# Performance work log

Hardware: AMD Instinct MI355X
Metric: run time of the kernel (lower is better)

Reference implementation:

```python
import jax, jax.numpy as jnp
import numpy as np

H = 1024
NH = 16
HD = H // NH

def setup_inputs() -> dict:
    key = jax.random.key(0)
    ks = jax.random.split(key, 8)
    s = 1.0 / np.sqrt(H)
    hidden_states = jax.random.normal(ks[0], (2, 2048, H), dtype=jnp.float32)
    attention_mask = jnp.zeros((2, 1, 1, 2048), dtype=jnp.float32)
    Wq = jax.random.uniform(ks[1], (H, H), jnp.float32, -s, s)
    bq = jax.random.uniform(ks[2], (H,), jnp.float32, -s, s)
    Wk = jax.random.uniform(ks[3], (H, H), jnp.float32, -s, s)
    bk = jax.random.uniform(ks[4], (H,), jnp.float32, -s, s)
    Wv = jax.random.uniform(ks[5], (H, H), jnp.float32, -s, s)
    bv = jax.random.uniform(ks[6], (H,), jnp.float32, -s, s)
    return {"hidden_states": hidden_states, "attention_mask": attention_mask,
            "Wq": Wq, "bq": bq, "Wk": Wk, "bk": bk, "Wv": Wv, "bv": bv}

def _split_heads(x):
    B, L, _ = x.shape
    return x.reshape(B, L, NH, HD).transpose(0, 2, 1, 3)  # [B, nh, L, hd]

def reference(hidden_states, attention_mask, Wq, bq, Wk, bk, Wv, bv):
    # QKV projections (nn.Linear: x @ W.T + b)
    Q = _split_heads(hidden_states @ Wq.T + bq)
    K = _split_heads(hidden_states @ Wk.T + bk)
    V = _split_heads(hidden_states @ Wv.T + bv)
    scale = 1.0 / np.sqrt(HD)
    scores = jnp.einsum('bhqd,bhkd->bhqk', Q, K) * scale  # [B, nh, L, L]
    scores = scores + attention_mask
    probs = jax.nn.softmax(scores, axis=-1)  # dropout in eval mode = identity
    context = jnp.einsum('bhqk,bhkd->bhqd', probs, V)
    B, _, L, _ = context.shape
    return context.transpose(0, 2, 1, 3).reshape(B, L, H)
```

## Files before the change

### kernel.cpp

```cpp
#include <hip/hip_runtime.h>
#include <math.h>
#include <stdint.h>

#define H_DIM 1024
#define NH 16
#define HD 64
#define B_DIM 2
#define L_DIM 2048
#define M_TOT (B_DIM * L_DIM)

typedef __bf16 bf16_t;
typedef __bf16 bf16x8 __attribute__((ext_vector_type(8)));
typedef __bf16 bf16x4 __attribute__((ext_vector_type(4)));
typedef float  f32x4  __attribute__((ext_vector_type(4)));

#define AS1 const __attribute__((address_space(1))) void*
#define AS3 __attribute__((address_space(3))) void*

__global__ __launch_bounds__(256)
void cast_all(const float* __restrict__ x,
              const float* __restrict__ Wq, const float* __restrict__ Wk,
              const float* __restrict__ Wv, bf16_t* __restrict__ dst)
{
    const size_t idx = ((size_t)blockIdx.x * 256 + threadIdx.x) * 4;
    const float* src;
    size_t off;
    if (idx < (size_t)M_TOT * H_DIM) { src = x; off = idx; }
    else {
        size_t j = idx - (size_t)M_TOT * H_DIM;
        int z = (int)(j >> 20);
        off = j & ((1u << 20) - 1);
        src = (z == 0) ? Wq : (z == 1) ? Wk : Wv;
    }
    const float4 v = *(const float4*)(src + off);
    bf16x4 o;
    o[0] = (bf16_t)v.x; o[1] = (bf16_t)v.y;
    o[2] = (bf16_t)v.z; o[3] = (bf16_t)v.w;
    *(bf16x4*)(dst + idx) = o;
}

__global__ __launch_bounds__(256, 1)
void qkv_mfma(const bf16_t* __restrict__ xb, const bf16_t* __restrict__ wb,
              const float* __restrict__ bq, const float* __restrict__ bk,
              const float* __restrict__ bv,
              bf16_t* __restrict__ qb, bf16_t* __restrict__ kb,
              bf16_t* __restrict__ vt)
{
    __shared__ bf16_t As0[128 * 32];
    __shared__ bf16_t As1[128 * 32];
    __shared__ bf16_t As2[128 * 32];
    __shared__ bf16_t Bs0[3][128 * 32];
    __shared__ bf16_t Bs1[3][128 * 32];
    __shared__ bf16_t Bs2[3][128 * 32];

    const int tid = threadIdx.x;
    const int n   = blockIdx.x;
    const int bn  = (n & 7) * 128;
    const int bm  = (n >> 3) * 128;

    const int wave = tid >> 6;
    const int lane = tid & 63;
    const int lc   = lane & 15;
    const int quad = lane >> 4;
    const int wm   = wave >> 1;
    const int wn   = wave & 1;

    f32x4 acc[3][4][4];
    #pragma unroll
    for (int z = 0; z < 3; ++z)
        #pragma unroll
        for (int i = 0; i < 4; ++i)
            #pragma unroll
            for (int j = 0; j < 4; ++j)
                acc[z][i][j] = (f32x4){0.f, 0.f, 0.f, 0.f};

    const int srow = tid >> 2;
    const int sseg = tid & 3;
    const bf16_t* gA = xb + (size_t)(bm + srow) * H_DIM + (sseg ^ (srow & 3)) * 8;
    const bf16_t* gB = wb + (size_t)(bn + srow) * H_DIM + (sseg ^ (srow & 3)) * 8;
    const int woff = wave * 1024;

    auto stage = [&](int k0, bf16_t* A_, bf16_t (*B_)[128 * 32]) {
        __builtin_amdgcn_global_load_lds((AS1)(gA + k0),
            (AS3)((char*)A_ + woff), 16, 0, 0);
        __builtin_amdgcn_global_load_lds((AS1)(gA + k0 + (size_t)64 * H_DIM),
            (AS3)((char*)A_ + woff + 4096), 16, 0, 0);
        #pragma unroll
        for (int z = 0; z < 3; ++z) {
            const bf16_t* g = gB + (size_t)z * H_DIM * H_DIM + k0;
            __builtin_amdgcn_global_load_lds((AS1)(g),
                (AS3)((char*)B_[z] + woff), 16, 0, 0);
            __builtin_amdgcn_global_load_lds((AS1)(g + (size_t)64 * H_DIM),
                (AS3)((char*)B_[z] + woff + 4096), 16, 0, 0);
        }
    };

    const int slot = (quad ^ (lc & 3)) * 8;
    auto compute = [&](const bf16_t* A_, const bf16_t (*B_)[128 * 32]) {
        bf16x8 a[4];
        #pragma unroll
        for (int mi = 0; mi < 4; ++mi)
            a[mi] = *(const bf16x8*)(A_ + (wm * 64 + mi * 16 + lc) * 32 + slot);
        #pragma unroll
        for (int z = 0; z < 3; ++z) {
            bf16x8 b[4];
            #pragma unroll
            for (int ni = 0; ni < 4; ++ni)
                b[ni] = *(const bf16x8*)(B_[z] + (wn * 64 + ni * 16 + lc) * 32 + slot);
            #pragma unroll
            for (int mi = 0; mi < 4; ++mi)
                #pragma unroll
                for (int ni = 0; ni < 4; ++ni)
                    acc[z][mi][ni] = __builtin_amdgcn_mfma_f32_16x16x32_bf16(
                        a[mi], b[ni], acc[z][mi][ni], 0, 0, 0);
        }
    };

    auto step = [&](int kk, bf16_t* cA, bf16_t (*cB)[128 * 32],
                    bf16_t* nA, bf16_t (*nB)[128 * 32], bool doStage) {
        __builtin_amdgcn_s_waitcnt(0x0F78);
        __builtin_amdgcn_s_barrier();
        if (doStage) stage((kk + 2) * 32, nA, nB);
        compute(cA, cB);
    };

    stage(0,  As0, Bs0);
    stage(32, As1, Bs1);
    #pragma unroll 1
    for (int t = 0; t < 10; ++t) {
        const int kk = t * 3;
        step(kk,     As0, Bs0, As2, Bs2, true);
        step(kk + 1, As1, Bs1, As0, Bs0, true);
        step(kk + 2, As2, Bs2, As1, Bs1, true);
    }
    step(30, As0, Bs0, As2, Bs2, false);
    __builtin_amdgcn_s_waitcnt(0x0F70);
    __builtin_amdgcn_s_barrier();
    compute(As1, Bs1);

    const int nb = bn + wn * 64;
    #pragma unroll
    for (int z = 0; z < 3; ++z) {
        const float* bias = (z == 0) ? bq : (z == 1) ? bk : bv;
        float biasv[4];
        #pragma unroll
        for (int ni = 0; ni < 4; ++ni) biasv[ni] = bias[nb + ni * 16 + lc];

        #pragma unroll
        for (int mi = 0; mi < 4; ++mi) {
            const int m0 = bm + wm * 64 + mi * 16 + quad * 4;
            if (z == 2) {
                const int b_ = m0 >> 11;
                const int l0 = m0 & 2047;
                #pragma unroll
                for (int ni = 0; ni < 4; ++ni) {
                    const int nn = nb + ni * 16 + lc;
                    const int h = nn >> 6, d = nn & 63;
                    bf16x4 pk;
                    #pragma unroll
                    for (int r = 0; r < 4; ++r)
                        pk[r] = (bf16_t)(acc[z][mi][ni][r] + biasv[ni]);
                    *(bf16x4*)(vt + (((size_t)(b_ * NH + h)) * HD + d) * L_DIM + l0) = pk;
                }
            } else {
                bf16_t* dst = (z == 0) ? qb : kb;
                #pragma unroll
                for (int r = 0; r < 4; ++r) {
                    const int m  = m0 + r;
                    const int b_ = m >> 11;
                    const int l  = m & 2047;
                    #pragma unroll
                    for (int ni = 0; ni < 4; ++ni) {
                        const int nn = nb + ni * 16 + lc;
                        const int h = nn >> 6, d = nn & 63;
                        dst[(((size_t)(b_ * NH + h)) * L_DIM + l) * HD + d] =
                            (bf16_t)(acc[z][mi][ni][r] + biasv[ni]);
                    }
                }
            }
        }
    }
}

#define EXP_C   0.180336879f
#define LOG2E   1.442695041f
#define EXP_SH  11.541560327f

__device__ __forceinline__ void attn_tile32(
    int kbase, bool pre,
    const bf16_t* curK, const bf16_t* curV,
    bf16_t* nxtK, bf16_t* nxtV,
    const bf16_t* gKw, const bf16_t* gVw, int wo,
    bf16_t* Ps, const float* mrow, int lc, int quad,
    const bf16x8 (&bQ)[2][2], f32x4 (&o)[2][4], float (&rs)[2])
{
    __builtin_amdgcn_s_waitcnt(0x0F70);
    __builtin_amdgcn_s_barrier();

    const int e = lc & 7;

    bf16x8 kf[2][2];
    #pragma unroll
    for (int ni = 0; ni < 2; ++ni) {
        const bf16_t* p = curK + (ni * 16 + lc) * 64;
        kf[ni][0] = *(const bf16x8*)(p + ((quad ^ e) << 3));
        kf[ni][1] = *(const bf16x8*)(p + (((quad ^ e) ^ 4) << 3));
    }

    if (pre) {
        const int nk = kbase + 32;
        #pragma unroll
        for (int i = 0; i < 2; ++i) {
            __builtin_amdgcn_global_load_lds(
                (AS1)(gKw + (size_t)nk * 64 + i * 512),
                (AS3)(nxtK + wo + i * 512), 16, 0, 0);
            __builtin_amdgcn_global_load_lds(
                (AS1)(gVw + nk + (size_t)i * 32768),
                (AS3)(nxtV + wo + i * 512), 16, 0, 0);
        }
    }

    float mvs[2][4];
    #pragma unroll
    for (int ni = 0; ni < 2; ++ni) {
        const float4 mv = *(const float4*)(mrow + kbase + ni * 16 + quad * 4);
        mvs[ni][0] = mv.x * LOG2E - EXP_SH;
        mvs[ni][1] = mv.y * LOG2E - EXP_SH;
        mvs[ni][2] = mv.z * LOG2E - EXP_SH;
        mvs[ni][3] = mv.w * LOG2E - EXP_SH;
    }

    #pragma unroll
    for (int f = 0; f < 2; ++f) {
        f32x4 s[2];
        #pragma unroll
        for (int ni = 0; ni < 2; ++ni) {
            f32x4 t = (f32x4){0.f, 0.f, 0.f, 0.f};
            t = __builtin_amdgcn_mfma_f32_16x16x32_bf16(kf[ni][0], bQ[f][0], t, 0, 0, 0);
            t = __builtin_amdgcn_mfma_f32_16x16x32_bf16(kf[ni][1], bQ[f][1], t, 0, 0, 0);
            s[ni] = t;
        }
        float acc = 0.f;
        #pragma unroll
        for (int ni = 0; ni < 2; ++ni) {
            bf16x4 pk;
            #pragma unroll
            for (int r = 0; r < 4; ++r) {
                const float p = __builtin_amdgcn_exp2f(s[ni][r] * EXP_C + mvs[ni][r]);
                acc += p;
                pk[r] = (bf16_t)p;
            }
            const int c = f * 4 + ni * 2 + (quad >> 1);
            *(bf16x4*)(Ps + lc * 64 + ((c ^ e) << 3) + ((quad & 1) << 2)) = pk;
        }
        rs[f] += acc;
    }

    bf16x8 vf[4];
    const int e2 = lc >> 1;
    #pragma unroll
    for (int dg = 0; dg < 4; ++dg) {
        const int p  = dg * 8 + (lc >> 1);
        const int ch = (((lc & 1) << 2) + quad) ^ e2;
        vf[dg] = *(const bf16x8*)(curV + p * 64 + (ch << 3));
    }

    #pragma unroll
    for (int f = 0; f < 2; ++f) {
        const int c = f * 4 + quad;
        const bf16x8 bP = *(const bf16x8*)(Ps + lc * 64 + ((c ^ e) << 3));
        #pragma unroll
        for (int dg = 0; dg < 4; ++dg)
            o[f][dg] = __builtin_amdgcn_mfma_f32_16x16x32_bf16(vf[dg], bP, o[f][dg], 0, 0, 0);
    }
}

__global__ __launch_bounds__(128, 4)
void attn_mfma(const bf16_t* __restrict__ qb, const bf16_t* __restrict__ kb,
               const bf16_t* __restrict__ vt, const float* __restrict__ mask,
               float* __restrict__ out, float* __restrict__ o1,
               float* __restrict__ l0, float* __restrict__ l1)
{
    __shared__ bf16_t Ks0[32 * 64];
    __shared__ bf16_t Ks1[32 * 64];
    __shared__ bf16_t Vs0[32 * 64];
    __shared__ bf16_t Vs1[32 * 64];
    __shared__ bf16_t Ps[2][16 * 64];

    const int tid  = threadIdx.x;
    const int wave = tid >> 6;
    const int lane = tid & 63;
    const int lc   = lane & 15;
    const int quad = lane >> 4;
    const int rl   = lane >> 3;
    const int sg   = lane & 7;

    const int n    = blockIdx.x;
    const int bh   = (n & 7) * 4 + ((n >> 3) & 3);
    const int q0   = ((n >> 5) & 31) * 64 + wave * 32;
    const int kh   = (n >> 10) & 1;
    const int k0   = kh << 10;
    const int b_   = bh >> 4;
    const int h    = bh & 15;

    bf16_t* Psw = Ps[wave];

    bf16x8 bQ[2][2];
    #pragma unroll
    for (int f = 0; f < 2; ++f) {
        const bf16_t* Qp = qb + ((size_t)bh * L_DIM + q0 + f * 16 + lc) * HD + quad * 8;
        bQ[f][0] = *(const bf16x8*)(Qp);
        bQ[f][1] = *(const bf16x8*)(Qp + 32);
    }

    const bf16_t* Kbase = kb + (size_t)bh * L_DIM * HD;
    const bf16_t* Vbase = vt + (size_t)bh * HD * L_DIM;
    const float*  mrow  = mask + (size_t)b_ * L_DIM + k0;

    const int cV = sg ^ rl;
    const bf16_t* gKw = Kbase + (size_t)(k0 + rl) * 64 + (sg ^ rl) * 8
                      + (size_t)wave * 1024;
    const bf16_t* gVw = Vbase + k0 + (size_t)(rl * 2 + (cV >> 2)) * L_DIM
                      + (cV & 3) * 8 + (size_t)wave * 65536;
    const int wo = wave * 1024;

    f32x4 o[2][4];
    #pragma unroll
    for (int f = 0; f < 2; ++f)
        #pragma unroll
        for (int dg = 0; dg < 4; ++dg) o[f][dg] = (f32x4){0.f, 0.f, 0.f, 0.f};
    float rs[2] = {0.f, 0.f};

    #pragma unroll
    for (int i = 0; i < 2; ++i) {
        __builtin_amdgcn_global_load_lds(
            (AS1)(gKw + i * 512),
            (AS3)(Ks0 + wo + i * 512), 16, 0, 0);
        __builtin_amdgcn_global_load_lds(
            (AS1)(gVw + (size_t)i * 32768),
            (AS3)(Vs0 + wo + i * 512), 16, 0, 0);
    }

    #pragma unroll 1
    for (int t2 = 0; t2 < 16; ++t2) {
        const int kb0 = t2 * 64;
        attn_tile32(kb0,      true,     Ks0, Vs0, Ks1, Vs1, gKw, gVw, wo, Psw,
                    mrow, lc, quad, bQ, o, rs);
        attn_tile32(kb0 + 32, t2 < 15,  Ks1, Vs1, Ks0, Vs0, gKw, gVw, wo, Psw,
                    mrow, lc, quad, bQ, o, rs);
    }

    float* obase = (kh == 0) ? out : o1;
    float* lbase = (kh == 0) ? l0  : l1;
    #pragma unroll
    for (int f = 0; f < 2; ++f) {
        float l = rs[f];
        l += __shfl_xor(l, 16);
        l += __shfl_xor(l, 32);
        if (quad == 0)
            lbase[(size_t)bh * L_DIM + q0 + f * 16 + lc] = l;
        float* orow = obase + ((size_t)(b_ * L_DIM + q0 + f * 16 + lc)) * H_DIM
                    + h * HD + quad * 4;
        #pragma unroll
        for (int dg = 0; dg < 4; ++dg)
            *(f32x4*)(orow + dg * 16) = o[f][dg];
    }
}

__global__ __launch_bounds__(256)
void attn_combine(const float* __restrict__ o1,
                  const float* __restrict__ l0, const float* __restrict__ l1,
                  float* __restrict__ out)
{
    const size_t idx = ((size_t)blockIdx.x * 256 + threadIdx.x) * 4;
    const int m   = (int)(idx >> 10);
    const int col = (int)(idx & 1023);
    const int b_  = m >> 11;
    const int q   = m & 2047;
    const int h   = col >> 6;
    const size_t lidx = ((size_t)(b_ * NH + h)) * L_DIM + q;
    const float inv = 1.0f / (l0[lidx] + l1[lidx]);
    f32x4 a = *(const f32x4*)(out + idx);
    const f32x4 b = *(const f32x4*)(o1 + idx);
    a = (a + b) * inv;
    *(f32x4*)(out + idx) = a;
}

extern "C" void kernel_launch(void* const* d_in, const int* in_sizes, int n_in,
                              void* d_out, int out_size, void* d_ws, size_t ws_size,
                              hipStream_t stream) {
    const float* hidden = (const float*)d_in[0];
    const float* mask   = (const float*)d_in[1];
    const float* Wq     = (const float*)d_in[2];
    const float* bq     = (const float*)d_in[3];
    const float* Wk     = (const float*)d_in[4];
    const float* bk     = (const float*)d_in[5];
    const float* Wv     = (const float*)d_in[6];
    const float* bv     = (const float*)d_in[7];
    float* out = (float*)d_out;

    const size_t XN = (size_t)M_TOT * H_DIM;
    const size_t WN = (size_t)3 * H_DIM * H_DIM;
    bf16_t* xwb = (bf16_t*)d_ws;
    bf16_t* qb  = xwb + XN + WN;
    bf16_t* kb  = qb + XN;
    bf16_t* vt  = kb + XN;
    float*  o1  = (float*)(vt + XN);
    float*  l0  = o1 + XN;
    float*  l1  = l0 + (size_t)B_DIM * NH * L_DIM;

    cast_all<<<(int)((XN + WN) / 1024), 256, 0, stream>>>(hidden, Wq, Wk, Wv, xwb);

    qkv_mfma<<<256, 256, 0, stream>>>(xwb, xwb + XN, bq, bk, bv, qb, kb, vt);

    attn_mfma<<<2048, 128, 0, stream>>>(qb, kb, vt, mask, out, o1, l0, l1);

    attn_combine<<<4096, 256, 0, stream>>>(o1, l0, l1, out);
}
```

Measured before the change: 177.5 us.

## Widen attention blocks to four waves sharing K/V tiles and LDS mask

New measurement: 172.2 us. 1.03x faster.

```diff
diff --git a/kernel.cpp b/kernel.cpp
--- a/kernel.cpp
+++ b/kernel.cpp
@@ -191,7 +191,7 @@
     const bf16_t* curK, const bf16_t* curV,
     bf16_t* nxtK, bf16_t* nxtV,
     const bf16_t* gKw, const bf16_t* gVw, int wo,
-    bf16_t* Ps, const float* mrow, int lc, int quad,
+    bf16_t* Ps, const float* mvsL, int lc, int quad,
     const bf16x8 (&bQ)[2][2], f32x4 (&o)[2][4], float (&rs)[2])
 {
     __builtin_amdgcn_s_waitcnt(0x0F70);
@@ -209,30 +209,23 @@
 
     if (pre) {
         const int nk = kbase + 32;
-        #pragma unroll
-        for (int i = 0; i < 2; ++i) {
-            __builtin_amdgcn_global_load_lds(
-                (AS1)(gKw + (size_t)nk * 64 + i * 512),
-                (AS3)(nxtK + wo + i * 512), 16, 0, 0);
-            __builtin_amdgcn_global_load_lds(
-                (AS1)(gVw + nk + (size_t)i * 32768),
-                (AS3)(nxtV + wo + i * 512), 16, 0, 0);
-        }
-    }
-
-    float mvs[2][4];
-    #pragma unroll
-    for (int ni = 0; ni < 2; ++ni) {
-        const float4 mv = *(const float4*)(mrow + kbase + ni * 16 + quad * 4);
-        mvs[ni][0] = mv.x * LOG2E - EXP_SH;
-        mvs[ni][1] = mv.y * LOG2E - EXP_SH;
-        mvs[ni][2] = mv.z * LOG2E - EXP_SH;
-        mvs[ni][3] = mv.w * LOG2E - EXP_SH;
-    }
+        __builtin_amdgcn_global_load_lds(
+            (AS1)(gKw + (size_t)nk * 64),
+            (AS3)(nxtK + wo), 16, 0, 0);
+        __builtin_amdgcn_global_load_lds(
+            (AS1)(gVw + nk),
+            (AS3)(nxtV + wo), 16, 0, 0);
+    }
+
+    f32x4 mvs[2];
+    #pragma unroll
+    for (int ni = 0; ni < 2; ++ni)
+        mvs[ni] = *(const f32x4*)(mvsL + kbase + ni * 16 + quad * 4);
 
     #pragma unroll
     for (int f = 0; f < 2; ++f) {
         f32x4 s[2];
+        __builtin_amdgcn_s_setprio(1);
         #pragma unroll
         for (int ni = 0; ni < 2; ++ni) {
             f32x4 t = (f32x4){0.f, 0.f, 0.f, 0.f};
@@ -240,6 +233,7 @@
             t = __builtin_amdgcn_mfma_f32_16x16x32_bf16(kf[ni][1], bQ[f][1], t, 0, 0, 0);
             s[ni] = t;
         }
+        __builtin_amdgcn_s_setprio(0);
         float acc = 0.f;
         #pragma unroll
         for (int ni = 0; ni < 2; ++ni) {
@@ -269,13 +263,15 @@
     for (int f = 0; f < 2; ++f) {
         const int c = f * 4 + quad;
         const bf16x8 bP = *(const bf16x8*)(Ps + lc * 64 + ((c ^ e) << 3));
+        __builtin_amdgcn_s_setprio(1);
         #pragma unroll
         for (int dg = 0; dg < 4; ++dg)
             o[f][dg] = __builtin_amdgcn_mfma_f32_16x16x32_bf16(vf[dg], bP, o[f][dg], 0, 0, 0);
-    }
-}
-
-__global__ __launch_bounds__(128, 4)
+        __builtin_amdgcn_s_setprio(0);
+    }
+}
+
+__global__ __launch_bounds__(256, 4)
 void attn_mfma(const bf16_t* __restrict__ qb, const bf16_t* __restrict__ kb,
                const bf16_t* __restrict__ vt, const float* __restrict__ mask,
                float* __restrict__ out, float* __restrict__ o1,
@@ -285,7 +281,8 @@
     __shared__ bf16_t Ks1[32 * 64];
     __shared__ bf16_t Vs0[32 * 64];
     __shared__ bf16_t Vs1[32 * 64];
-    __shared__ bf16_t Ps[2][16 * 64];
+    __shared__ bf16_t Ps[4][16 * 64];
+    __shared__ float  Ms[1024];
 
     const int tid  = threadIdx.x;
     const int wave = tid >> 6;
@@ -297,9 +294,9 @@
 
     const int n    = blockIdx.x;
     const int bh   = (n & 7) * 4 + ((n >> 3) & 3);
-    const int q0   = ((n >> 5) & 31) * 64 + wave * 32;
-    const int kh   = (n >> 10) & 1;
-    const int k0   = kh << 10;
+    const int q0   = ((n >> 5) & 15) * 128 + wave * 32;
+    const int ks   = (n >> 9) & 1;
+    const int k0   = ks << 10;
     const int b_   = bh >> 4;
     const int h    = bh & 15;
 
@@ -317,12 +314,22 @@
     const bf16_t* Vbase = vt + (size_t)bh * HD * L_DIM;
     const float*  mrow  = mask + (size_t)b_ * L_DIM + k0;
 
+    {
+        const float4 m4 = *(const float4*)(mrow + tid * 4);
+        f32x4 w;
+        w[0] = m4.x * LOG2E - EXP_SH;
+        w[1] = m4.y * LOG2E - EXP_SH;
+        w[2] = m4.z * LOG2E - EXP_SH;
+        w[3] = m4.w * LOG2E - EXP_SH;
+        *(f32x4*)(Ms + tid * 4) = w;
+    }
+
     const int cV = sg ^ rl;
-    const bf16_t* gKw = Kbase + (size_t)(k0 + rl) * 64 + (sg ^ rl) * 8
-                      + (size_t)wave * 1024;
-    const bf16_t* gVw = Vbase + k0 + (size_t)(rl * 2 + (cV >> 2)) * L_DIM
-                      + (cV & 3) * 8 + (size_t)wave * 65536;
-    const int wo = wave * 1024;
+    const bf16_t* gKw = Kbase + (size_t)(k0 + wave * 8 + rl) * 64 + (sg ^ rl) * 8;
+    const bf16_t* gVw = Vbase + k0
+                      + (size_t)(wave * 16 + rl * 2 + (cV >> 2)) * L_DIM
+                      + (cV & 3) * 8;
+    const int wo = wave * 512;
 
     f32x4 o[2][4];
     #pragma unroll
@@ -331,27 +338,22 @@
         for (int dg = 0; dg < 4; ++dg) o[f][dg] = (f32x4){0.f, 0.f, 0.f, 0.f};
     float rs[2] = {0.f, 0.f};
 
-    #pragma unroll
-    for (int i = 0; i < 2; ++i) {
-        __builtin_amdgcn_global_load_lds(
-            (AS1)(gKw + i * 512),
-            (AS3)(Ks0 + wo + i * 512), 16, 0, 0);
-        __builtin_amdgcn_global_load_lds(
-            (AS1)(gVw + (size_t)i * 32768),
-            (AS3)(Vs0 + wo + i * 512), 16, 0, 0);
-    }
+    __builtin_amdgcn_global_load_lds((AS1)(gKw), (AS3)(Ks0 + wo), 16, 0, 0);
+    __builtin_amdgcn_global_load_lds((AS1)(gVw), (AS3)(Vs0 + wo), 16, 0, 0);
+
+    __syncthreads();
 
     #pragma unroll 1
     for (int t2 = 0; t2 < 16; ++t2) {
         const int kb0 = t2 * 64;
         attn_tile32(kb0,      true,     Ks0, Vs0, Ks1, Vs1, gKw, gVw, wo, Psw,
-                    mrow, lc, quad, bQ, o, rs);
+                    Ms, lc, quad, bQ, o, rs);
         attn_tile32(kb0 + 32, t2 < 15,  Ks1, Vs1, Ks0, Vs0, gKw, gVw, wo, Psw,
-                    mrow, lc, quad, bQ, o, rs);
-    }
-
-    float* obase = (kh == 0) ? out : o1;
-    float* lbase = (kh == 0) ? l0  : l1;
+                    Ms, lc, quad, bQ, o, rs);
+    }
+
+    float* obase = (ks == 0) ? out : o1;
+    float* lbase = (ks == 0) ? l0  : l1;
     #pragma unroll
     for (int f = 0; f < 2; ++f) {
         float l = rs[f];
@@ -413,7 +415,7 @@
 
     qkv_mfma<<<256, 256, 0, stream>>>(xwb, xwb + XN, bq, bk, bv, qb, kb, vt);
 
-    attn_mfma<<<2048, 128, 0, stream>>>(qb, kb, vt, mask, out, o1, l0, l1);
+    attn_mfma<<<1024, 256, 0, stream>>>(qb, kb, vt, mask, out, o1, l0, l1);
 
     attn_combine<<<4096, 256, 0, stream>>>(o1, l0, l1, out);
 }
```
